# Kernel optimization log

Hardware: AMD Instinct MI355X
Metric: run time of the kernel (lower is better)

The kernel has to match this reference:

```python
import jax, jax.numpy as jnp
import numpy as np
from jax import lax

DIM = 1024      # model dim
DS = 16         # d_state
DC = 4          # d_conv
EXP = 2
DI = DIM * EXP  # d_inner = 2048
B, L = 2, 1024


def setup_inputs() -> dict:
    key = jax.random.key(0)
    ks = jax.random.split(key, 10)
    s = lambda k, shape, sc: jax.random.normal(k, shape, jnp.float32) * sc
    return {
        "x": s(ks[0], (B, L, DIM), 1.0),
        "norm_w": jnp.ones((DIM,), jnp.float32),
        "norm_b": jnp.zeros((DIM,), jnp.float32),
        "in_proj_w": s(ks[1], (2 * DI, DIM), DIM ** -0.5),
        "conv_w": s(ks[2], (DI, 1, DC), DC ** -0.5),   # depthwise: (out=DI, in/groups=1, K)
        "conv_b": jnp.zeros((DI,), jnp.float32),
        "x_proj_w": s(ks[3], (2 * DS + 1, DI), DI ** -0.5),
        "dt_w": s(ks[4], (DI, 1), 1.0),
        "dt_b": jax.random.uniform(ks[5], (DI,), jnp.float32, -0.001, 0.001),
        "A_log": s(ks[6], (DI, DS), 1.0),              # self.A (randn); A = -exp(A_log)
        "D_skip": jnp.ones((DI,), jnp.float32),
        "out_proj_w": s(ks[7], (DIM, DI), DI ** -0.5),
    }


def _ssm(x, x_proj_w, dt_w, dt_b, A_log, D_skip):
    # x: (B, L, DI)
    xp = jnp.einsum('bli,pi->blp', x, x_proj_w)            # (B, L, 2*DS+1)
    delta = jax.nn.softplus(xp[..., :1] * dt_w[:, 0] + dt_b)  # (B, L, DI)
    Bp = xp[..., 1:DS + 1]                                  # (B, L, DS)
    Cp = xp[..., DS + 1:]                                   # (B, L, DS)
    A = -jnp.exp(A_log)                                     # (DI, DS)
    dA = jnp.exp(delta[..., None] * A)                      # (B, L, DI, DS)
    dB = delta[..., None] * Bp[:, :, None, :] * x[..., None]  # (B, L, DI, DS)

    def step(h, inp):
        dA_t, dB_t, C_t = inp                               # (B,DI,DS),(B,DI,DS),(B,DS)
        h = dA_t * h + dB_t
        return h, jnp.einsum('bdn,bn->bd', h, C_t)

    h0 = jnp.zeros((x.shape[0], DI, DS), x.dtype)
    _, ys = lax.scan(step, h0, (jnp.swapaxes(dA, 0, 1),
                                jnp.swapaxes(dB, 0, 1),
                                jnp.swapaxes(Cp, 0, 1)))
    y = jnp.swapaxes(ys, 0, 1)                              # (B, L, DI)
    return y + x * D_skip


def reference(x, norm_w, norm_b, in_proj_w, conv_w, conv_b,
              x_proj_w, dt_w, dt_b, A_log, D_skip, out_proj_w):
    # LayerNorm
    mu = x.mean(-1, keepdims=True)
    var = ((x - mu) ** 2).mean(-1, keepdims=True)
    xn = (x - mu) * lax.rsqrt(var + 1e-5) * norm_w + norm_b
    # input projection and gate split
    xz = jnp.einsum('bld,pd->blp', xn, in_proj_w)           # (B, L, 2*DI)
    xi, z = xz[..., :DI], xz[..., DI:]
    # causal depthwise conv (torch pads K-1 both sides then slices [:L] == left-pad K-1)
    xc = lax.conv_general_dilated(jnp.swapaxes(xi, 1, 2), conv_w, (1,),
                                  [(DC - 1, 0)], feature_group_count=DI,
                                  dimension_numbers=('NCH', 'OIH', 'NCH'))
    xc = jnp.swapaxes(xc + conv_b[None, :, None], 1, 2)     # (B, L, DI)
    xc = jax.nn.silu(xc)
    y = _ssm(xc, x_proj_w, dt_w, dt_b, A_log, D_skip)
    y = y * jax.nn.silu(z)
    return x + jnp.einsum('bli,di->bld', y, out_proj_w)
```

## Files before the change

kernel.cpp:

```cpp
#include <hip/hip_runtime.h>
#include <stdint.h>

#define BATCH 2
#define SEQ   1024
#define DIM_  1024
#define DS_   16
#define DI_   2048
#define NTOK  (BATCH*SEQ)
#define NSEG  32
#define LSEG  (SEQ/NSEG)

typedef unsigned short u16;
using s16x8 = __attribute__((ext_vector_type(8))) short;
using f32x4 = __attribute__((ext_vector_type(4))) float;
using u16x4 = __attribute__((ext_vector_type(4))) unsigned short;
using u16x8 = __attribute__((ext_vector_type(8))) unsigned short;

__device__ __forceinline__ float bf2f(u16 u) {
  union { unsigned int i; float f; } c; c.i = ((unsigned int)u) << 16; return c.f;
}
__device__ __forceinline__ u16 f2bf(float f) {
  union { float f; unsigned int i; } c; c.f = f;
  unsigned int r = c.i + 0x7fffu + ((c.i >> 16) & 1u);
  return (u16)(r >> 16);
}
__device__ __forceinline__ float softplus_f(float x) {
  return (x > 15.f) ? x : __logf(1.f + __expf(x));
}

__global__ __launch_bounds__(256) void cvt_pad_kernel(const float* __restrict__ a,
    u16* __restrict__ o) {
  int i = blockIdx.x * 256 + threadIdx.x;
  if (i >= 32768) return;
  int p = (i * 4) >> 11;
  u16x4 r;
  if (p < 33) {
    float4 v = ((const float4*)a)[i];
    r[0] = f2bf(v.x); r[1] = f2bf(v.y); r[2] = f2bf(v.z); r[3] = f2bf(v.w);
  } else {
    r[0] = 0; r[1] = 0; r[2] = 0; r[3] = 0;
  }
  ((u16x4*)o)[i] = r;
}

__global__ __launch_bounds__(256) void ln_kernel(const float* __restrict__ x,
    const float* __restrict__ w, const float* __restrict__ b, u16* __restrict__ xn) {
  int t = blockIdx.x, tid = threadIdx.x;
  const float* row = x + (size_t)t * DIM_;
  float4 v = ((const float4*)row)[tid];
  float f[4] = {v.x, v.y, v.z, v.w};
  float s = 0.f, sq = 0.f;
#pragma unroll
  for (int j = 0; j < 4; j++) { s += f[j]; sq += f[j] * f[j]; }
#pragma unroll
  for (int m = 1; m < 64; m <<= 1) { s += __shfl_xor(s, m); sq += __shfl_xor(sq, m); }
  __shared__ float rs_[4], rq_[4];
  int wv = tid >> 6;
  if ((tid & 63) == 0) { rs_[wv] = s; rq_[wv] = sq; }
  __syncthreads();
  s = rs_[0] + rs_[1] + rs_[2] + rs_[3];
  sq = rq_[0] + rq_[1] + rq_[2] + rq_[3];
  float mu = s * (1.0f / DIM_);
  float var = sq * (1.0f / DIM_) - mu * mu;
  float rstd = rsqrtf(var + 1e-5f);
  float4 wn = ((const float4*)w)[tid];
  float4 bn = ((const float4*)b)[tid];
  u16x4 o;
  o[0] = f2bf((f[0] - mu) * rstd * wn.x + bn.x);
  o[1] = f2bf((f[1] - mu) * rstd * wn.y + bn.y);
  o[2] = f2bf((f[2] - mu) * rstd * wn.z + bn.z);
  o[3] = f2bf((f[3] - mu) * rstd * wn.w + bn.w);
  *(u16x4*)(xn + (size_t)t * DIM_ + tid * 4) = o;
}

template<int TBM, int TBN, typename OUT, int EPI, int WF32, int KSPLIT = 1>
__global__ __launch_bounds__(256) void gemm_bt(const u16* __restrict__ A,
    const void* __restrict__ Wt_, OUT* __restrict__ C, const float* __restrict__ X,
    int M, int N, int K) {
  constexpr int BK = 32;
  constexpr int LDT = BK + 8;
  constexpr int WM = TBM / 2, WN = TBN / 2;
  constexpr int MI = WM / 16, NJ = WN / 16;
  constexpr int ALn = TBM / 64, BLn = TBN / 64;
  __shared__ __align__(16) u16 sA[TBM * LDT];
  __shared__ __align__(16) u16 sB[TBN * LDT];
  const int tid = threadIdx.x;
  const int lane = tid & 63, wv = tid >> 6;
  const int wm = (wv >> 1) * WM, wn = (wv & 1) * WN;
  const int bm0 = blockIdx.y * TBM, bn0 = blockIdx.x * TBN;
  const int q = lane >> 4, r16 = lane & 15;
  const int srow = tid >> 2, scol = (tid & 3) * 8;
  const int kc = K / KSPLIT;
  const int k0 = (KSPLIT > 1) ? blockIdx.z * kc : 0;
  const int kend = k0 + kc;

  f32x4 acc[MI][NJ];
#pragma unroll
  for (int i = 0; i < MI; i++)
#pragma unroll
    for (int j = 0; j < NJ; j++)
#pragma unroll
      for (int r = 0; r < 4; r++) acc[i][j][r] = 0.f;

  const u16* Ag = A + (size_t)bm0 * K + scol + k0;
  const u16* Wgh = (const u16*)Wt_ + (size_t)bn0 * K + scol + k0;
  const float* Wgf = (const float*)Wt_ + (size_t)bn0 * K + scol + k0;
  s16x8 ra[ALn], rb[BLn];
  float4 rbf[BLn][2];
#pragma unroll
  for (int i = 0; i < ALn; i++) ra[i] = *(const s16x8*)(Ag + (size_t)(srow + i * 64) * K);
  if constexpr (WF32) {
#pragma unroll
    for (int i = 0; i < BLn; i++) {
      const float* p = Wgf + (size_t)(srow + i * 64) * K;
      rbf[i][0] = *(const float4*)p;
      rbf[i][1] = *(const float4*)(p + 4);
    }
  } else {
#pragma unroll
    for (int i = 0; i < BLn; i++) rb[i] = *(const s16x8*)(Wgh + (size_t)(srow + i * 64) * K);
  }

  for (int kt = k0; kt < kend; kt += BK) {
    __syncthreads();
#pragma unroll
    for (int i = 0; i < ALn; i++) *(s16x8*)&sA[(srow + i * 64) * LDT + scol] = ra[i];
    if constexpr (WF32) {
#pragma unroll
      for (int i = 0; i < BLn; i++) {
        u16x8 wb;
        wb[0] = f2bf(rbf[i][0].x); wb[1] = f2bf(rbf[i][0].y);
        wb[2] = f2bf(rbf[i][0].z); wb[3] = f2bf(rbf[i][0].w);
        wb[4] = f2bf(rbf[i][1].x); wb[5] = f2bf(rbf[i][1].y);
        wb[6] = f2bf(rbf[i][1].z); wb[7] = f2bf(rbf[i][1].w);
        *(u16x8*)&sB[(srow + i * 64) * LDT + scol] = wb;
      }
    } else {
#pragma unroll
      for (int i = 0; i < BLn; i++) *(s16x8*)&sB[(srow + i * 64) * LDT + scol] = rb[i];
    }
    __syncthreads();
    int kn = kt + BK - k0;
    if (kn < kc) {
#pragma unroll
      for (int i = 0; i < ALn; i++) ra[i] = *(const s16x8*)(Ag + (size_t)(srow + i * 64) * K + kn);
      if constexpr (WF32) {
#pragma unroll
        for (int i = 0; i < BLn; i++) {
          const float* p = Wgf + (size_t)(srow + i * 64) * K + kn;
          rbf[i][0] = *(const float4*)p;
          rbf[i][1] = *(const float4*)(p + 4);
        }
      } else {
#pragma unroll
        for (int i = 0; i < BLn; i++) rb[i] = *(const s16x8*)(Wgh + (size_t)(srow + i * 64) * K + kn);
      }
    }
    s16x8 fa[MI], fb[NJ];
#pragma unroll
    for (int i = 0; i < MI; i++) fa[i] = *(const s16x8*)&sA[(wm + i * 16 + r16) * LDT + q * 8];
#pragma unroll
    for (int j = 0; j < NJ; j++) fb[j] = *(const s16x8*)&sB[(wn + j * 16 + r16) * LDT + q * 8];
#pragma unroll
    for (int i = 0; i < MI; i++)
#pragma unroll
      for (int j = 0; j < NJ; j++)
        acc[i][j] = __builtin_amdgcn_mfma_f32_16x16x32_bf16(fa[i], fb[j], acc[i][j], 0, 0, 0);
  }
  OUT* Cz = C + ((KSPLIT > 1) ? (size_t)blockIdx.z * M * N : 0);
#pragma unroll
  for (int i = 0; i < MI; i++)
#pragma unroll
    for (int j = 0; j < NJ; j++) {
      int row0 = bm0 + wm + i * 16 + q * 4;
      int col = bn0 + wn + j * 16 + r16;
#pragma unroll
      for (int r = 0; r < 4; r++) {
        size_t off = (size_t)(row0 + r) * N + col;
        float v = acc[i][j][r];
        if constexpr (EPI == 1) v += X[off];
        if constexpr (sizeof(OUT) == 2) Cz[off] = f2bf(v);
        else                            Cz[off] = v;
      }
    }
}

__global__ __launch_bounds__(256) void reduce_xp_kernel(const float* __restrict__ part,
    float* __restrict__ xp) {
  int g = blockIdx.x * 256 + threadIdx.x;
  constexpr size_t STR = (size_t)NTOK * 64;
  float s = 0.f;
#pragma unroll
  for (int k = 0; k < 8; k++) s += part[(size_t)k * STR + g];
  xp[g] = s;
}

__global__ __launch_bounds__(256) void conv_silu_kernel(const u16* __restrict__ xz,
    const float* __restrict__ cw, const float* __restrict__ cb, u16* __restrict__ xc) {
  int t = blockIdx.x;
  int l = t & (SEQ - 1);
  int c0 = threadIdx.x * 8;
  float acc[8], wk[8][4];
#pragma unroll
  for (int j = 0; j < 8; j++) {
    float4 wv = ((const float4*)cw)[c0 + j];
    wk[j][0] = wv.x; wk[j][1] = wv.y; wk[j][2] = wv.z; wk[j][3] = wv.w;
    acc[j] = cb[c0 + j];
  }
#pragma unroll
  for (int k = 0; k < 4; k++) {
    int lk = l - 3 + k;
    if (lk >= 0) {
      u16x8 v = *(const u16x8*)(xz + (size_t)(t - 3 + k) * (2 * DI_) + c0);
#pragma unroll
      for (int j = 0; j < 8; j++) acc[j] = fmaf(bf2f(v[j]), wk[j][k], acc[j]);
    }
  }
  u16x8 o;
#pragma unroll
  for (int j = 0; j < 8; j++) {
    float a = acc[j];
    o[j] = f2bf(a / (1.0f + __expf(-a)));
  }
  *(u16x8*)(xc + (size_t)t * DI_ + c0) = o;
}

__global__ __launch_bounds__(256) void delta_bc_kernel(const float* __restrict__ xp,
    const float* __restrict__ dtw, const float* __restrict__ dtb,
    u16* __restrict__ xz, float* __restrict__ bc) {
  int t = blockIdx.x;
  int tid = threadIdx.x;
  int c0 = tid * 8;
  float dr = xp[(size_t)t * 64];
  float wv[8], bv[8];
  *(float4*)wv = ((const float4*)(dtw + c0))[0];
  *(float4*)(wv + 4) = ((const float4*)(dtw + c0))[1];
  *(float4*)bv = ((const float4*)(dtb + c0))[0];
  *(float4*)(bv + 4) = ((const float4*)(dtb + c0))[1];
  u16x8 o;
#pragma unroll
  for (int j = 0; j < 8; j++) o[j] = f2bf(softplus_f(dr * wv[j] + bv[j]));
  *(u16x8*)(xz + (size_t)t * (2 * DI_) + c0) = o;
  if (tid < 32) bc[(size_t)t * 32 + tid] = xp[(size_t)t * 64 + 1 + tid];
}

__global__ __launch_bounds__(256) void scan_pass1(const float* __restrict__ bc,
    const u16* __restrict__ dlt, const u16* __restrict__ xc,
    const float* __restrict__ A_log, float* __restrict__ P, float* __restrict__ Q) {
  int tid = threadIdx.x;
  int lane = tid & 63, wv = tid >> 6;
  int nl = (lane & 3) * 4;
  int d = blockIdx.x * 64 + wv * 16 + (lane >> 2);
  int s = blockIdx.y, b = blockIdx.z;
  int t0 = b * SEQ + s * LSEG;
  float4 Ain = *(const float4*)(A_log + d * DS_ + nl);
  f32x4 Av;
  Av[0] = -__expf(Ain.x); Av[1] = -__expf(Ain.y);
  Av[2] = -__expf(Ain.z); Av[3] = -__expf(Ain.w);
  f32x4 Pv, h;
#pragma unroll
  for (int i = 0; i < 4; i++) { Pv[i] = 1.f; h[i] = 0.f; }
#pragma unroll 4
  for (int j = 0; j < LSEG; j++) {
    int t = t0 + j;
    float delta = bf2f(dlt[(size_t)t * (2 * DI_) + d]);
    float xcv = bf2f(xc[(size_t)t * DI_ + d]);
    float4 B4 = *(const float4*)(bc + (size_t)t * 32 + nl);
    float du = delta * xcv;
#pragma unroll
    for (int i = 0; i < 4; i++) {
      float a = __expf(delta * Av[i]);
      Pv[i] *= a;
      float bi = (i == 0) ? B4.x : (i == 1) ? B4.y : (i == 2) ? B4.z : B4.w;
      h[i] = fmaf(a, h[i], du * bi);
    }
  }
  size_t idx = ((size_t)((b * NSEG + s) * DI_ + d)) * 16 + nl;
  *(f32x4*)(P + idx) = Pv;
  *(f32x4*)(Q + idx) = h;
}

__global__ __launch_bounds__(256) void scan_combine(const float* __restrict__ P,
    float* __restrict__ Q) {
  int g = blockIdx.x * 256 + threadIdx.x;
  int n = g & 15, d = (g >> 4) & (DI_ - 1), b = g >> 15;
  size_t base = ((size_t)b * NSEG * DI_ + d) * 16 + n;
  constexpr size_t STR = (size_t)DI_ * 16;
  float p_[NSEG], q_[NSEG];
#pragma unroll
  for (int s = 0; s < NSEG; s++) {
    p_[s] = P[base + s * STR];
    q_[s] = Q[base + s * STR];
  }
  float hh = 0.f;
#pragma unroll
  for (int s = 0; s < NSEG; s++) {
    Q[base + s * STR] = hh;
    hh = fmaf(p_[s], hh, q_[s]);
  }
}

__global__ __launch_bounds__(256) void scan_pass2(const float* __restrict__ bc,
    const u16* __restrict__ dlt, const u16* __restrict__ xc,
    const float* __restrict__ A_log, const float* __restrict__ Hin,
    u16* __restrict__ yb) {
  int tid = threadIdx.x;
  int lane = tid & 63, wv = tid >> 6;
  int nl = (lane & 3) * 4;
  int d = blockIdx.x * 64 + wv * 16 + (lane >> 2);
  int s = blockIdx.y, b = blockIdx.z;
  int t0 = b * SEQ + s * LSEG;
  float4 Ain = *(const float4*)(A_log + d * DS_ + nl);
  f32x4 Av;
  Av[0] = -__expf(Ain.x); Av[1] = -__expf(Ain.y);
  Av[2] = -__expf(Ain.z); Av[3] = -__expf(Ain.w);
  size_t idx = ((size_t)((b * NSEG + s) * DI_ + d)) * 16 + nl;
  f32x4 h = *(const f32x4*)(Hin + idx);
#pragma unroll 4
  for (int j = 0; j < LSEG; j++) {
    int t = t0 + j;
    float delta = bf2f(dlt[(size_t)t * (2 * DI_) + d]);
    float xcv = bf2f(xc[(size_t)t * DI_ + d]);
    float4 B4 = *(const float4*)(bc + (size_t)t * 32 + nl);
    float4 C4 = *(const float4*)(bc + (size_t)t * 32 + 16 + nl);
    float du = delta * xcv;
#pragma unroll
    for (int i = 0; i < 4; i++) {
      float a = __expf(delta * Av[i]);
      float bi = (i == 0) ? B4.x : (i == 1) ? B4.y : (i == 2) ? B4.z : B4.w;
      h[i] = fmaf(a, h[i], du * bi);
    }
    float p = h[0] * C4.x;
    p = fmaf(h[1], C4.y, p);
    p = fmaf(h[2], C4.z, p);
    p = fmaf(h[3], C4.w, p);
    p += __shfl_xor(p, 1);
    p += __shfl_xor(p, 2);
    if ((lane & 3) == 0) yb[(size_t)t * DI_ + d] = f2bf(p);
  }
}

__global__ __launch_bounds__(256) void gate_kernel(u16* __restrict__ yb,
    const u16* __restrict__ xc, const u16* __restrict__ xz,
    const float* __restrict__ Dskip) {
  int t = blockIdx.x;
  int c0 = threadIdx.x * 8;
  u16x8 pv = *(const u16x8*)(yb + (size_t)t * DI_ + c0);
  u16x8 xcv = *(const u16x8*)(xc + (size_t)t * DI_ + c0);
  u16x8 zv = *(const u16x8*)(xz + (size_t)t * (2 * DI_) + DI_ + c0);
  float Dv[8];
  *(float4*)Dv = ((const float4*)(Dskip + c0))[0];
  *(float4*)(Dv + 4) = ((const float4*)(Dskip + c0))[1];
  u16x8 o;
#pragma unroll
  for (int j = 0; j < 8; j++) {
    float z = bf2f(zv[j]);
    float sz = z / (1.0f + __expf(-z));
    o[j] = f2bf((bf2f(pv[j]) + bf2f(xcv[j]) * Dv[j]) * sz);
  }
  *(u16x8*)(yb + (size_t)t * DI_ + c0) = o;
}

extern "C" void kernel_launch(void* const* d_in, const int* in_sizes, int n_in,
                              void* d_out, int out_size, void* d_ws, size_t ws_size,
                              hipStream_t stream) {
  const float* x      = (const float*)d_in[0];
  const float* norm_w = (const float*)d_in[1];
  const float* norm_b = (const float*)d_in[2];
  const float* in_w   = (const float*)d_in[3];
  const float* conv_w = (const float*)d_in[4];
  const float* conv_b = (const float*)d_in[5];
  const float* xproj_w= (const float*)d_in[6];
  const float* dt_w   = (const float*)d_in[7];
  const float* dt_b   = (const float*)d_in[8];
  const float* A_log  = (const float*)d_in[9];
  const float* D_skip = (const float*)d_in[10];
  const float* out_w  = (const float*)d_in[11];
  float* out = (float*)d_out;

  char* ws = (char*)d_ws;
  size_t off = 0;
  auto alloc = [&](size_t bytes) { void* p = ws + off; off += (bytes + 255) & ~255ULL; return p; };
  u16* xpw_bf = (u16*)alloc((size_t)64 * DI_ * 2);
  u16* xz     = (u16*)alloc((size_t)NTOK * 2 * DI_ * 2);
  u16* xc     = (u16*)alloc((size_t)NTOK * DI_ * 2);
  float* xp   = (float*)alloc((size_t)NTOK * 64 * 4);
  float* bc   = (float*)alloc((size_t)NTOK * 32 * 4);
  char* regionA = (char*)alloc((size_t)BATCH * NSEG * DI_ * 16 * 4);
  float* Q = (float*)alloc((size_t)BATCH * NSEG * DI_ * 16 * 4);
  u16* xn   = (u16*)regionA;
  float* P  = (float*)regionA;
  u16* yb   = (u16*)regionA;
  float* xp_part = Q;

  cvt_pad_kernel<<<128, 256, 0, stream>>>(xproj_w, xpw_bf);
  ln_kernel<<<NTOK, 256, 0, stream>>>(x, norm_w, norm_b, xn);
  gemm_bt<128, 64, u16, 0, 1><<<dim3((2 * DI_) / 64, NTOK / 128), 256, 0, stream>>>(
      xn, in_w, xz, nullptr, NTOK, 2 * DI_, DIM_);
  conv_silu_kernel<<<NTOK, 256, 0, stream>>>(xz, conv_w, conv_b, xc);
  gemm_bt<64, 64, float, 0, 0, 8><<<dim3(1, NTOK / 64, 8), 256, 0, stream>>>(
      xc, xpw_bf, xp_part, nullptr, NTOK, 64, DI_);
  reduce_xp_kernel<<<NTOK * 64 / 256, 256, 0, stream>>>(xp_part, xp);
  delta_bc_kernel<<<NTOK, 256, 0, stream>>>(xp, dt_w, dt_b, xz, bc);
  scan_pass1<<<dim3(DI_ / 64, NSEG, BATCH), 256, 0, stream>>>(bc, xz, xc, A_log, P, Q);
  scan_combine<<<BATCH * DI_ * 16 / 256, 256, 0, stream>>>(P, Q);
  scan_pass2<<<dim3(DI_ / 64, NSEG, BATCH), 256, 0, stream>>>(bc, xz, xc, A_log, Q, yb);
  gate_kernel<<<NTOK, 256, 0, stream>>>(yb, xc, xz, D_skip);
  gemm_bt<64, 64, float, 1, 1><<<dim3(DIM_ / 64, NTOK / 64), 256, 0, stream>>>(
      yb, out_w, out, x, NTOK, DIM_, DI_);
}
```

Measured before the change: 253.6 us.

## Parameterize GEMM K-tile depth and split-K the output projection

The GEMM template now takes the K-tile depth BK as a parameter, with the load mapping and inner MFMA loop generalized to cover several 32-wide k-steps per tile. The input projection and the output projection now use BK=64, which halves barrier and loop overhead per K. The output projection is split into two K halves written to a scratch buffer that reuses the xz region, and a new reduce kernel adds the partials and the residual x. This doubles the number of blocks for the narrow output GEMM to improve occupancy, at the cost of an extra pass through global memory and one more launch.

```diff
diff --git a/kernel.cpp b/kernel.cpp
--- a/kernel.cpp
+++ b/kernel.cpp
@@ -73,15 +73,18 @@
   *(u16x4*)(xn + (size_t)t * DIM_ + tid * 4) = o;
 }
 
-template<int TBM, int TBN, typename OUT, int EPI, int WF32, int KSPLIT = 1>
+template<int TBM, int TBN, int BK, typename OUT, int EPI, int WF32, int KSPLIT = 1>
 __global__ __launch_bounds__(256) void gemm_bt(const u16* __restrict__ A,
     const void* __restrict__ Wt_, OUT* __restrict__ C, const float* __restrict__ X,
     int M, int N, int K) {
-  constexpr int BK = 32;
   constexpr int LDT = BK + 8;
+  constexpr int TPR = BK / 8;
+  constexpr int RPP = 256 / TPR;
+  constexpr int ALn = TBM / RPP;
+  constexpr int BLn = TBN / RPP;
+  constexpr int KK = BK / 32;
   constexpr int WM = TBM / 2, WN = TBN / 2;
   constexpr int MI = WM / 16, NJ = WN / 16;
-  constexpr int ALn = TBM / 64, BLn = TBN / 64;
   __shared__ __align__(16) u16 sA[TBM * LDT];
   __shared__ __align__(16) u16 sB[TBN * LDT];
   const int tid = threadIdx.x;
@@ -89,7 +92,7 @@
   const int wm = (wv >> 1) * WM, wn = (wv & 1) * WN;
   const int bm0 = blockIdx.y * TBM, bn0 = blockIdx.x * TBN;
   const int q = lane >> 4, r16 = lane & 15;
-  const int srow = tid >> 2, scol = (tid & 3) * 8;
+  const int srow = tid / TPR, scol = (tid % TPR) * 8;
   const int kc = K / KSPLIT;
   const int k0 = (KSPLIT > 1) ? blockIdx.z * kc : 0;
   const int kend = k0 + kc;
@@ -108,23 +111,23 @@
   s16x8 ra[ALn], rb[BLn];
   float4 rbf[BLn][2];
 #pragma unroll
-  for (int i = 0; i < ALn; i++) ra[i] = *(const s16x8*)(Ag + (size_t)(srow + i * 64) * K);
+  for (int i = 0; i < ALn; i++) ra[i] = *(const s16x8*)(Ag + (size_t)(srow + i * RPP) * K);
   if constexpr (WF32) {
 #pragma unroll
     for (int i = 0; i < BLn; i++) {
-      const float* p = Wgf + (size_t)(srow + i * 64) * K;
+      const float* p = Wgf + (size_t)(srow + i * RPP) * K;
       rbf[i][0] = *(const float4*)p;
       rbf[i][1] = *(const float4*)(p + 4);
     }
   } else {
 #pragma unroll
-    for (int i = 0; i < BLn; i++) rb[i] = *(const s16x8*)(Wgh + (size_t)(srow + i * 64) * K);
+    for (int i = 0; i < BLn; i++) rb[i] = *(const s16x8*)(Wgh + (size_t)(srow + i * RPP) * K);
   }
 
   for (int kt = k0; kt < kend; kt += BK) {
     __syncthreads();
 #pragma unroll
-    for (int i = 0; i < ALn; i++) *(s16x8*)&sA[(srow + i * 64) * LDT + scol] = ra[i];
+    for (int i = 0; i < ALn; i++) *(s16x8*)&sA[(srow + i * RPP) * LDT + scol] = ra[i];
     if constexpr (WF32) {
 #pragma unroll
       for (int i = 0; i < BLn; i++) {
@@ -133,39 +136,44 @@
         wb[2] = f2bf(rbf[i][0].z); wb[3] = f2bf(rbf[i][0].w);
         wb[4] = f2bf(rbf[i][1].x); wb[5] = f2bf(rbf[i][1].y);
         wb[6] = f2bf(rbf[i][1].z); wb[7] = f2bf(rbf[i][1].w);
-        *(u16x8*)&sB[(srow + i * 64) * LDT + scol] = wb;
+        *(u16x8*)&sB[(srow + i * RPP) * LDT + scol] = wb;
       }
     } else {
 #pragma unroll
-      for (int i = 0; i < BLn; i++) *(s16x8*)&sB[(srow + i * 64) * LDT + scol] = rb[i];
+      for (int i = 0; i < BLn; i++) *(s16x8*)&sB[(srow + i * RPP) * LDT + scol] = rb[i];
     }
     __syncthreads();
     int kn = kt + BK - k0;
     if (kn < kc) {
 #pragma unroll
-      for (int i = 0; i < ALn; i++) ra[i] = *(const s16x8*)(Ag + (size_t)(srow + i * 64) * K + kn);
+      for (int i = 0; i < ALn; i++) ra[i] = *(const s16x8*)(Ag + (size_t)(srow + i * RPP) * K + kn);
       if constexpr (WF32) {
 #pragma unroll
         for (int i = 0; i < BLn; i++) {
-          const float* p = Wgf + (size_t)(srow + i * 64) * K + kn;
+          const float* p = Wgf + (size_t)(srow + i * RPP) * K + kn;
           rbf[i][0] = *(const float4*)p;
           rbf[i][1] = *(const float4*)(p + 4);
         }
       } else {
 #pragma unroll
-        for (int i = 0; i < BLn; i++) rb[i] = *(const s16x8*)(Wgh + (size_t)(srow + i * 64) * K + kn);
+        for (int i = 0; i < BLn; i++) rb[i] = *(const s16x8*)(Wgh + (size_t)(srow + i * RPP) * K + kn);
       }
     }
-    s16x8 fa[MI], fb[NJ];
-#pragma unroll
-    for (int i = 0; i < MI; i++) fa[i] = *(const s16x8*)&sA[(wm + i * 16 + r16) * LDT + q * 8];
-#pragma unroll
-    for (int j = 0; j < NJ; j++) fb[j] = *(const s16x8*)&sB[(wn + j * 16 + r16) * LDT + q * 8];
-#pragma unroll
-    for (int i = 0; i < MI; i++)
+#pragma unroll
+    for (int kk = 0; kk < KK; kk++) {
+      s16x8 fa[MI], fb[NJ];
+#pragma unroll
+      for (int i = 0; i < MI; i++)
+        fa[i] = *(const s16x8*)&sA[(wm + i * 16 + r16) * LDT + kk * 32 + q * 8];
 #pragma unroll
       for (int j = 0; j < NJ; j++)
-        acc[i][j] = __builtin_amdgcn_mfma_f32_16x16x32_bf16(fa[i], fb[j], acc[i][j], 0, 0, 0);
+        fb[j] = *(const s16x8*)&sB[(wn + j * 16 + r16) * LDT + kk * 32 + q * 8];
+#pragma unroll
+      for (int i = 0; i < MI; i++)
+#pragma unroll
+        for (int j = 0; j < NJ; j++)
+          acc[i][j] = __builtin_amdgcn_mfma_f32_16x16x32_bf16(fa[i], fb[j], acc[i][j], 0, 0, 0);
+    }
   }
   OUT* Cz = C + ((KSPLIT > 1) ? (size_t)blockIdx.z * M * N : 0);
 #pragma unroll
@@ -193,6 +201,21 @@
 #pragma unroll
   for (int k = 0; k < 8; k++) s += part[(size_t)k * STR + g];
   xp[g] = s;
+}
+
+__global__ __launch_bounds__(256) void reduce_out_kernel(const float* __restrict__ part,
+    const float* __restrict__ x, float* __restrict__ out) {
+  int g = blockIdx.x * 256 + threadIdx.x;
+  constexpr size_t STR = (size_t)NTOK * DIM_ / 4;
+  float4 a = ((const float4*)part)[g];
+  float4 b = ((const float4*)part)[g + STR];
+  float4 xv = ((const float4*)x)[g];
+  float4 o;
+  o.x = xv.x + a.x + b.x;
+  o.y = xv.y + a.y + b.y;
+  o.z = xv.z + a.z + b.z;
+  o.w = xv.w + a.w + b.w;
+  ((float4*)out)[g] = o;
 }
 
 __global__ __launch_bounds__(256) void conv_silu_kernel(const u16* __restrict__ xz,
@@ -392,13 +415,14 @@
   float* P  = (float*)regionA;
   u16* yb   = (u16*)regionA;
   float* xp_part = Q;
+  float* out_part = (float*)xz;
 
   cvt_pad_kernel<<<128, 256, 0, stream>>>(xproj_w, xpw_bf);
   ln_kernel<<<NTOK, 256, 0, stream>>>(x, norm_w, norm_b, xn);
-  gemm_bt<128, 64, u16, 0, 1><<<dim3((2 * DI_) / 64, NTOK / 128), 256, 0, stream>>>(
+  gemm_bt<128, 64, 64, u16, 0, 1><<<dim3((2 * DI_) / 64, NTOK / 128), 256, 0, stream>>>(
       xn, in_w, xz, nullptr, NTOK, 2 * DI_, DIM_);
   conv_silu_kernel<<<NTOK, 256, 0, stream>>>(xz, conv_w, conv_b, xc);
-  gemm_bt<64, 64, float, 0, 0, 8><<<dim3(1, NTOK / 64, 8), 256, 0, stream>>>(
+  gemm_bt<64, 64, 32, float, 0, 0, 8><<<dim3(1, NTOK / 64, 8), 256, 0, stream>>>(
       xc, xpw_bf, xp_part, nullptr, NTOK, 64, DI_);
   reduce_xp_kernel<<<NTOK * 64 / 256, 256, 0, stream>>>(xp_part, xp);
   delta_bc_kernel<<<NTOK, 256, 0, stream>>>(xp, dt_w, dt_b, xz, bc);
@@ -406,6 +430,7 @@
   scan_combine<<<BATCH * DI_ * 16 / 256, 256, 0, stream>>>(P, Q);
   scan_pass2<<<dim3(DI_ / 64, NSEG, BATCH), 256, 0, stream>>>(bc, xz, xc, A_log, Q, yb);
   gate_kernel<<<NTOK, 256, 0, stream>>>(yb, xc, xz, D_skip);
-  gemm_bt<64, 64, float, 1, 1><<<dim3(DIM_ / 64, NTOK / 64), 256, 0, stream>>>(
-      yb, out_w, out, x, NTOK, DIM_, DI_);
-}
+  gemm_bt<64, 64, 64, float, 0, 1, 2><<<dim3(DIM_ / 64, NTOK / 64, 2), 256, 0, stream>>>(
+      yb, out_w, out_part, nullptr, NTOK, DIM_, DI_);
+  reduce_out_kernel<<<NTOK * DIM_ / 4 / 256, 256, 0, stream>>>(out_part, x, out);
+}
```

Measured after the change: 238.4 us. 6.0% less time.
